# Performance work log

Hardware: AMD Instinct MI355X
Metric: run time of the kernel (lower is better)

Reference implementation:

```python
import jax, jax.numpy as jnp
import numpy as np

B, N, D_MODEL, H, D_K, D_V = 4, 1024, 1024, 16, 64, 1024  # N == D_V required by the module's output matmul


def setup_inputs() -> dict:
    key = jax.random.key(0)
    ks = jax.random.split(key, 7)
    def xavier(k, shape):
        fan_in, fan_out = shape[-2], shape[-1]
        std = (2.0 / (fan_in + fan_out)) ** 0.5
        return jax.random.normal(k, shape, dtype=jnp.float32) * std
    return {
        "query": jax.random.normal(ks[0], (B, N, D_MODEL), dtype=jnp.float32),
        "key": jax.random.normal(ks[1], (B, N, D_MODEL), dtype=jnp.float32),
        "value": jax.random.normal(ks[2], (B, N, D_MODEL), dtype=jnp.float32),
        "w_q": xavier(ks[3], (H, D_MODEL, D_K)),
        "w_k": xavier(ks[4], (H, D_MODEL, D_K)),
        "w_v": xavier(ks[5], (H, D_MODEL, D_V)),
        "w_o": xavier(ks[6], (D_MODEL, H * D_V)),
    }


def reference(query, key, value, w_q, w_k, w_v, w_o):
    # Per-head projections: [B,N,d_model] x [H,d_model,d] -> [B,H,N,d]
    q = jnp.einsum('bnd,hdk->bhnk', query, w_q)
    k = jnp.einsum('bnd,hdk->bhnk', key, w_k)
    v = jnp.einsum('bnd,hdv->bhnv', value, w_v)
    scale = 1.0 / jnp.sqrt(jnp.asarray(q.shape[-1], q.dtype))
    scores = jnp.einsum('bhqk,bhmk->bhqm', q, k) * scale  # [B,H,N,N]
    weights = jax.nn.softmax(scores, axis=-1)
    out = jnp.einsum('bhqm,bhmv->bhqv', weights, v)  # [B,H,N,d_v]
    out = out.reshape(out.shape[0], -1, out.shape[-1])  # [B, H*N, d_v]
    # Faithful to source: torch.matmul(w_o, output) with w_o [d_model, H*d_v];
    # requires H*d_v == H*N (N == d_v); result [B, d_model, d_v].
    return jnp.einsum('de,bev->bdv', w_o, out)
```

## Files before the change

kernel.cpp:

```cpp
#include <hip/hip_runtime.h>
#include <hip/hip_bf16.h>

typedef __hip_bfloat16 bf16;
typedef __attribute__((ext_vector_type(8))) short short8;
typedef __attribute__((ext_vector_type(4))) float floatx4;

#define BK 64
#define LDK 72

__device__ __forceinline__ void gload_lds16(const void* g, void* l) {
    __builtin_amdgcn_global_load_lds(
        (const __attribute__((address_space(1))) void*)g,
        (__attribute__((address_space(3))) void*)l, 16, 0, 0);
}

template<bool OUT_BF16>
__global__ void __launch_bounds__(256) gemm_nt_lds(
    const bf16* __restrict__ A, const bf16* __restrict__ B, void* __restrict__ Cv,
    int M, int N, int K, int lda, int ldb, int ldc,
    long sA, long sB, long sC)
{
    __shared__ __align__(16) bf16 As[128 * 64];
    __shared__ __align__(16) bf16 Bs[128 * 64];

    int bx = blockIdx.x, by = blockIdx.y, bz = blockIdx.z;
    if (gridDim.x == 8 && gridDim.y == 8 && (gridDim.z & 7) == 0) {
        int hw  = bx + (by << 3) + (bz << 6);
        int xcd = hw & 7;
        int idx = hw >> 3;
        int zper = gridDim.z >> 3;
        bz = xcd * zper + (idx >> 6);
        int rem = idx & 63;
        by = rem >> 3;
        bx = rem & 7;
    }

    long aoff = (long)bz * sA;
    long boff = (long)bz * sB;
    long coff = (long)bz * sC;

    int m0 = by * 128;
    int n0 = bx * 128;
    int tid  = threadIdx.x;
    int lane = tid & 63;
    int wave = tid >> 6;
    int quad = lane >> 4;
    int l16  = lane & 15;
    int wm = (wave >> 1) * 64;
    int wn = (wave & 1) * 64;

    int lrow   = lane >> 3;
    int lchunk = (lane & 7) ^ lrow;
    int swz    = l16 & 7;

    const bf16* Abase = A + aoff + (long)m0 * lda;
    const bf16* Bbase = B + boff + (long)n0 * ldb;

    floatx4 acc[4][4] = {};
    const int nt = K / BK;

    for (int kt = 0; kt < nt; kt++) {
        __syncthreads();
        long kofs = (long)kt * BK;
#pragma unroll
        for (int s = 0; s < 4; s++) {
            int r = wave * 32 + s * 8;
            gload_lds16(Abase + (long)(r + lrow) * lda + kofs + lchunk * 8, &As[r * 64]);
            gload_lds16(Bbase + (long)(r + lrow) * ldb + kofs + lchunk * 8, &Bs[r * 64]);
        }
        __syncthreads();

#pragma unroll
        for (int ks = 0; ks < 2; ks++) {
            short8 af[4], bfr[4];
#pragma unroll
            for (int i = 0; i < 4; i++) {
                int ri = wm + i * 16 + l16;
                af[i] = *(const short8*)(&As[ri * 64 + (((ks << 2) | quad) ^ swz) * 8]);
            }
#pragma unroll
            for (int j = 0; j < 4; j++) {
                int rj = wn + j * 16 + l16;
                bfr[j] = *(const short8*)(&Bs[rj * 64 + (((ks << 2) | quad) ^ swz) * 8]);
            }
#pragma unroll
            for (int i = 0; i < 4; i++)
#pragma unroll
                for (int j = 0; j < 4; j++)
                    acc[i][j] = __builtin_amdgcn_mfma_f32_16x16x32_bf16(af[i], bfr[j], acc[i][j], 0, 0, 0);
        }
    }

#pragma unroll
    for (int i = 0; i < 4; i++) {
        int row = m0 + wm + i * 16 + quad * 4;
#pragma unroll
        for (int j = 0; j < 4; j++) {
            int col = n0 + wn + j * 16 + l16;
#pragma unroll
            for (int v = 0; v < 4; v++) {
                int r = row + v;
                float val = acc[i][j][v];
                if (OUT_BF16)
                    ((bf16*)Cv)[coff + (long)r * ldc + col] = __float2bfloat16(val);
                else
                    ((float*)Cv)[coff + (long)r * ldc + col] = val;
            }
        }
    }
}

template<bool OUT_BF16, bool A_F32, bool B_F32>
__global__ void __launch_bounds__(256) gemm_nt(
    const void* __restrict__ Av, const void* __restrict__ Bv, void* __restrict__ Cv,
    int M, int N, int K, int lda, int ldb, int ldc,
    long sA, long sB, long sC)
{
    __shared__ __align__(16) bf16 As[128 * LDK];
    __shared__ __align__(16) bf16 Bs[128 * LDK];

    int bx = blockIdx.x, by = blockIdx.y, bz = blockIdx.z;
    if (gridDim.x == 8 && gridDim.y == 8 && (gridDim.z & 7) == 0) {
        int hw  = bx + (by << 3) + (bz << 6);
        int xcd = hw & 7;
        int idx = hw >> 3;
        int zper = gridDim.z >> 3;
        bz = xcd * zper + (idx >> 6);
        int rem = idx & 63;
        by = rem >> 3;
        bx = rem & 7;
    }

    long aoff = (long)bz * sA;
    long boff = (long)bz * sB;
    long coff = (long)bz * sC;

    int m0 = by * 128;
    int n0 = bx * 128;
    int tid  = threadIdx.x;
    int lane = tid & 63;
    int wave = tid >> 6;
    int quad = lane >> 4;
    int l16  = lane & 15;
    int wm = (wave >> 1) * 64;
    int wn = (wave & 1) * 64;

    int sr = tid >> 3;
    int sc = (tid & 7) * 8;

    floatx4 acc[4][4] = {};

    uint4  pa[4], pb[4];
    float4 pa0[4], pa1[4], pb0[4], pb1[4];

    const int nt = K / BK;

#pragma unroll
    for (int s = 0; s < 4; s++) {
        int r = sr + 32 * s;
        int gm = m0 + r;
        if (A_F32) {
            const float* p = (const float*)Av + aoff + (long)gm * lda + sc;
            if (gm < M) { pa0[s] = *(const float4*)p; pa1[s] = *(const float4*)(p + 4); }
            else { pa0[s] = {0,0,0,0}; pa1[s] = {0,0,0,0}; }
        } else {
            pa[s] = (gm < M) ? *(const uint4*)((const bf16*)Av + aoff + (long)gm * lda + sc)
                             : (uint4){0,0,0,0};
        }
        int gn = n0 + r;
        if (B_F32) {
            const float* p = (const float*)Bv + boff + (long)gn * ldb + sc;
            if (gn < N) { pb0[s] = *(const float4*)p; pb1[s] = *(const float4*)(p + 4); }
            else { pb0[s] = {0,0,0,0}; pb1[s] = {0,0,0,0}; }
        } else {
            pb[s] = (gn < N) ? *(const uint4*)((const bf16*)Bv + boff + (long)gn * ldb + sc)
                             : (uint4){0,0,0,0};
        }
    }

    for (int kt = 0; kt < nt; kt++) {
        __syncthreads();
#pragma unroll
        for (int s = 0; s < 4; s++) {
            int r = sr + 32 * s;
            if (A_F32) {
                bf16 t[8];
                t[0]=__float2bfloat16(pa0[s].x); t[1]=__float2bfloat16(pa0[s].y);
                t[2]=__float2bfloat16(pa0[s].z); t[3]=__float2bfloat16(pa0[s].w);
                t[4]=__float2bfloat16(pa1[s].x); t[5]=__float2bfloat16(pa1[s].y);
                t[6]=__float2bfloat16(pa1[s].z); t[7]=__float2bfloat16(pa1[s].w);
                *(uint4*)(&As[r * LDK + sc]) = *(const uint4*)t;
            } else {
                *(uint4*)(&As[r * LDK + sc]) = pa[s];
            }
            if (B_F32) {
                bf16 t[8];
                t[0]=__float2bfloat16(pb0[s].x); t[1]=__float2bfloat16(pb0[s].y);
                t[2]=__float2bfloat16(pb0[s].z); t[3]=__float2bfloat16(pb0[s].w);
                t[4]=__float2bfloat16(pb1[s].x); t[5]=__float2bfloat16(pb1[s].y);
                t[6]=__float2bfloat16(pb1[s].z); t[7]=__float2bfloat16(pb1[s].w);
                *(uint4*)(&Bs[r * LDK + sc]) = *(const uint4*)t;
            } else {
                *(uint4*)(&Bs[r * LDK + sc]) = pb[s];
            }
        }
        __syncthreads();

        if (kt + 1 < nt) {
            int k0 = (kt + 1) * BK;
#pragma unroll
            for (int s = 0; s < 4; s++) {
                int r = sr + 32 * s;
                int gm = m0 + r;
                if (A_F32) {
                    const float* p = (const float*)Av + aoff + (long)gm * lda + k0 + sc;
                    if (gm < M) { pa0[s] = *(const float4*)p; pa1[s] = *(const float4*)(p + 4); }
                    else { pa0[s] = {0,0,0,0}; pa1[s] = {0,0,0,0}; }
                } else {
                    pa[s] = (gm < M) ? *(const uint4*)((const bf16*)Av + aoff + (long)gm * lda + k0 + sc)
                                     : (uint4){0,0,0,0};
                }
                int gn = n0 + r;
                if (B_F32) {
                    const float* p = (const float*)Bv + boff + (long)gn * ldb + k0 + sc;
                    if (gn < N) { pb0[s] = *(const float4*)p; pb1[s] = *(const float4*)(p + 4); }
                    else { pb0[s] = {0,0,0,0}; pb1[s] = {0,0,0,0}; }
                } else {
                    pb[s] = (gn < N) ? *(const uint4*)((const bf16*)Bv + boff + (long)gn * ldb + k0 + sc)
                                     : (uint4){0,0,0,0};
                }
            }
        }

#pragma unroll
        for (int ks = 0; ks < 2; ks++) {
            short8 af[4], bfr[4];
#pragma unroll
            for (int i = 0; i < 4; i++)
                af[i] = *(const short8*)(&As[(wm + i * 16 + l16) * LDK + ks * 32 + quad * 8]);
#pragma unroll
            for (int j = 0; j < 4; j++)
                bfr[j] = *(const short8*)(&Bs[(wn + j * 16 + l16) * LDK + ks * 32 + quad * 8]);
#pragma unroll
            for (int i = 0; i < 4; i++)
#pragma unroll
                for (int j = 0; j < 4; j++)
                    acc[i][j] = __builtin_amdgcn_mfma_f32_16x16x32_bf16(af[i], bfr[j], acc[i][j], 0, 0, 0);
        }
    }

#pragma unroll
    for (int i = 0; i < 4; i++) {
        int row = m0 + wm + i * 16 + quad * 4;
#pragma unroll
        for (int j = 0; j < 4; j++) {
            int col = n0 + wn + j * 16 + l16;
            if (col >= N) continue;
#pragma unroll
            for (int v = 0; v < 4; v++) {
                int r = row + v;
                if (r < M) {
                    float val = acc[i][j][v];
                    if (OUT_BF16)
                        ((bf16*)Cv)[coff + (long)r * ldc + col] = __float2bfloat16(val);
                    else
                        ((float*)Cv)[coff + (long)r * ldc + col] = val;
                }
            }
        }
    }
}

__global__ void __launch_bounds__(256) attn_softmax(
    const bf16* __restrict__ Q, const bf16* __restrict__ Kb, bf16* __restrict__ Wts)
{
    __shared__ __align__(16) bf16 Ks[64 * 72];

    int h = blockIdx.y;
    const bf16* Qbh = Q  + (long)h * 262144;
    const bf16* Kbh = Kb + (long)h * 262144;
    bf16* W = Wts + (long)h * 1048576;

    int tid  = threadIdx.x;
    int lane = tid & 63;
    int wave = tid >> 6;
    int quad = lane >> 4;
    int l16  = lane & 15;
    int q0 = blockIdx.x * 64 + wave * 16;

    short8 a0 = *(const short8*)(Qbh + (long)(q0 + l16) * 64 + quad * 8);
    short8 a1 = *(const short8*)(Qbh + (long)(q0 + l16) * 64 + 32 + quad * 8);

    int sr = tid >> 3;
    int sc = (tid & 7) * 8;

    const float scale = 0.125f;
    float m_v[4] = {-1e30f, -1e30f, -1e30f, -1e30f};
    float l_v[4] = {0.f, 0.f, 0.f, 0.f};

    for (int t = 0; t < 16; t++) {
        __syncthreads();
        const bf16* src = Kbh + (long)(t * 64 + sr) * 64 + sc;
        *(uint4*)(&Ks[sr * 72 + sc])        = *(const uint4*)src;
        *(uint4*)(&Ks[(sr + 32) * 72 + sc]) = *(const uint4*)(src + 32 * 64);
        __syncthreads();
#pragma unroll
        for (int j = 0; j < 4; j++) {
            short8 b0 = *(const short8*)(&Ks[(j * 16 + l16) * 72 + quad * 8]);
            short8 b1 = *(const short8*)(&Ks[(j * 16 + l16) * 72 + 32 + quad * 8]);
            floatx4 acc = {0.f, 0.f, 0.f, 0.f};
            acc = __builtin_amdgcn_mfma_f32_16x16x32_bf16(a0, b0, acc, 0, 0, 0);
            acc = __builtin_amdgcn_mfma_f32_16x16x32_bf16(a1, b1, acc, 0, 0, 0);
#pragma unroll
            for (int v = 0; v < 4; v++) {
                float s  = acc[v] * scale;
                float nm = fmaxf(m_v[v], s);
                l_v[v] = l_v[v] * __expf(m_v[v] - nm) + __expf(s - nm);
                m_v[v] = nm;
            }
        }
    }

#pragma unroll
    for (int d = 1; d < 16; d <<= 1) {
#pragma unroll
        for (int v = 0; v < 4; v++) {
            float om = __shfl_xor(m_v[v], d);
            float ol = __shfl_xor(l_v[v], d);
            float nm = fmaxf(m_v[v], om);
            l_v[v] = l_v[v] * __expf(m_v[v] - nm) + ol * __expf(om - nm);
            m_v[v] = nm;
        }
    }
    float linv[4];
#pragma unroll
    for (int v = 0; v < 4; v++) linv[v] = 1.0f / l_v[v];

    for (int t = 0; t < 16; t++) {
        __syncthreads();
        const bf16* src = Kbh + (long)(t * 64 + sr) * 64 + sc;
        *(uint4*)(&Ks[sr * 72 + sc])        = *(const uint4*)src;
        *(uint4*)(&Ks[(sr + 32) * 72 + sc]) = *(const uint4*)(src + 32 * 64);
        __syncthreads();
#pragma unroll
        for (int j = 0; j < 4; j++) {
            short8 b0 = *(const short8*)(&Ks[(j * 16 + l16) * 72 + quad * 8]);
            short8 b1 = *(const short8*)(&Ks[(j * 16 + l16) * 72 + 32 + quad * 8]);
            floatx4 acc = {0.f, 0.f, 0.f, 0.f};
            acc = __builtin_amdgcn_mfma_f32_16x16x32_bf16(a0, b0, acc, 0, 0, 0);
            acc = __builtin_amdgcn_mfma_f32_16x16x32_bf16(a1, b1, acc, 0, 0, 0);
#pragma unroll
            for (int v = 0; v < 4; v++) {
                float w = __expf(acc[v] * scale - m_v[v]) * linv[v];
                W[(long)(q0 + quad * 4 + v) * 1024 + t * 64 + j * 16 + l16] = __float2bfloat16(w);
            }
        }
    }
}

__global__ void __launch_bounds__(256) cast_bf16_k(
    const float* __restrict__ in, bf16* __restrict__ out, int n4)
{
    int i = blockIdx.x * 256 + threadIdx.x;
    if (i >= n4) return;
    float4 v = ((const float4*)in)[i];
    bf16 t[4] = {__float2bfloat16(v.x), __float2bfloat16(v.y),
                 __float2bfloat16(v.z), __float2bfloat16(v.w)};
    ((uint2*)out)[i] = *(const uint2*)t;
}

__global__ void __launch_bounds__(256) transpose_cast(
    const float* __restrict__ in, bf16* __restrict__ out, int R, int C)
{
    __shared__ float t[32][33];
    int h = blockIdx.z;
    const float* inh = in + (long)h * R * C;
    bf16* outh = out + (long)h * R * C;
    int c0 = blockIdx.x * 32, r0 = blockIdx.y * 32;
    int tx = threadIdx.x, ty = threadIdx.y;
#pragma unroll
    for (int i = 0; i < 32; i += 8)
        t[ty + i][tx] = inh[(long)(r0 + ty + i) * C + c0 + tx];
    __syncthreads();
#pragma unroll
    for (int i = 0; i < 32; i += 8)
        outh[(long)(c0 + ty + i) * R + r0 + tx] = __float2bfloat16(t[tx][ty + i]);
}

__global__ void __launch_bounds__(256) reduce16_k(
    const float* __restrict__ part, float* __restrict__ out)
{
    int i = blockIdx.x * 256 + threadIdx.x;
    float4 s = ((const float4*)part)[i];
#pragma unroll
    for (int c = 1; c < 16; c++) {
        float4 p = ((const float4*)part)[c * 262144 + i];
        s.x += p.x; s.y += p.y; s.z += p.z; s.w += p.w;
    }
    ((float4*)out)[i] = s;
}

extern "C" void kernel_launch(void* const* d_in, const int* in_sizes, int n_in,
                              void* d_out, int out_size, void* d_ws, size_t ws_size,
                              hipStream_t stream) {
    const float* query = (const float*)d_in[0];
    const float* key   = (const float*)d_in[1];
    const float* value = (const float*)d_in[2];
    const float* w_q   = (const float*)d_in[3];
    const float* w_k   = (const float*)d_in[4];
    const float* w_v   = (const float*)d_in[5];
    const float* w_o   = (const float*)d_in[6];
    float* out = (float*)d_out;

    char* ws = (char*)d_ws;
    const size_t MB = (size_t)1 << 20;
    bf16* wqt      = (bf16*)(ws + 0 * MB);
    bf16* wkt      = (bf16*)(ws + 2 * MB);
    bf16* wvt      = (bf16*)(ws + 4 * MB);
    bf16* wob      = (bf16*)(ws + 36 * MB);
    bf16* qb       = (bf16*)(ws + 68 * MB);
    bf16* kb       = (bf16*)(ws + 76 * MB);
    bf16* vt_b     = (bf16*)(ws + 84 * MB);
    bf16* wts_b    = (bf16*)(ws + 116 * MB);
    bf16* att_b    = (bf16*)(ws + 148 * MB);
    bf16* value_bf = (bf16*)(ws + 148 * MB);
    float* out_part = (float*)(ws + 84 * MB);

    transpose_cast<<<dim3(2, 32, 16),  dim3(32, 8), 0, stream>>>(w_q, wqt, 1024, 64);
    transpose_cast<<<dim3(2, 32, 16),  dim3(32, 8), 0, stream>>>(w_k, wkt, 1024, 64);
    transpose_cast<<<dim3(32, 32, 16), dim3(32, 8), 0, stream>>>(w_v, wvt, 1024, 1024);
    cast_bf16_k<<<16384, 256, 0, stream>>>(w_o, wob, 1024 * 16384 / 4);

    gemm_nt<true, true, false><<<dim3(1, 32, 16), 256, 0, stream>>>(
        query, wqt, qb, 4096, 64, 1024, 1024, 1024, 64, 0L, 65536L, 262144L);
    gemm_nt<true, true, false><<<dim3(1, 32, 16), 256, 0, stream>>>(
        key, wkt, kb, 4096, 64, 1024, 1024, 1024, 64, 0L, 65536L, 262144L);

    for (int b = 0; b < 4; b++) {
        cast_bf16_k<<<1024, 256, 0, stream>>>(value + (long)b * 1048576, value_bf, 262144);

        gemm_nt_lds<true><<<dim3(8, 8, 16), 256, 0, stream>>>(
            wvt, value_bf, vt_b,
            1024, 1024, 1024, 1024, 1024, 1024, 1048576L, 0L, 1048576L);

        attn_softmax<<<dim3(16, 16), 256, 0, stream>>>(
            qb + (long)b * 65536, kb + (long)b * 65536, wts_b);

        gemm_nt_lds<true><<<dim3(8, 8, 16), 256, 0, stream>>>(
            vt_b, wts_b, att_b,
            1024, 1024, 1024, 1024, 1024, 16384, 1048576L, 1048576L, 1024L);

        gemm_nt_lds<false><<<dim3(8, 8, 16), 256, 0, stream>>>(
            wob, att_b, out_part,
            1024, 1024, 1024, 16384, 16384, 1024, 1024L, 1024L, 1048576L);

        reduce16_k<<<1024, 256, 0, stream>>>(out_part, out + (long)b * 1048576);
    }

    (void)in_sizes; (void)n_in; (void)out_size; (void)ws_size;
}
```

Baseline: 1.016 ms.

## Use 256x256 double-buffered GEMM tiles with 512 threads for batched matmuls

Replaces the 128x128 single-buffered LDS GEMM with a 256x256 tile kernel of 8 waves. Each wave now computes 128x64, and the kernel double-buffers LDS so the next K-tile's global-to-LDS loads overlap the MFMAs. It raises MFMA priority with setprio and remaps blocks across XCDs for the new grid. The larger tiles raise data reuse per byte loaded but use 128KB of LDS per block, which gives only one block per CU and 256 blocks per launch. The XCD remap is also removed from the older gemm_nt kernel.

```diff
diff --git a/kernel.cpp b/kernel.cpp
--- a/kernel.cpp
+++ b/kernel.cpp
@@ -15,96 +15,101 @@
 }
 
 template<bool OUT_BF16>
-__global__ void __launch_bounds__(256) gemm_nt_lds(
+__global__ void __launch_bounds__(512) gemm_nt_256(
     const bf16* __restrict__ A, const bf16* __restrict__ B, void* __restrict__ Cv,
-    int M, int N, int K, int lda, int ldb, int ldc,
+    int K, int lda, int ldb, int ldc,
     long sA, long sB, long sC)
 {
-    __shared__ __align__(16) bf16 As[128 * 64];
-    __shared__ __align__(16) bf16 Bs[128 * 64];
+    __shared__ __align__(16) bf16 As[2][256 * 64];
+    __shared__ __align__(16) bf16 Bs[2][256 * 64];
 
     int bx = blockIdx.x, by = blockIdx.y, bz = blockIdx.z;
-    if (gridDim.x == 8 && gridDim.y == 8 && (gridDim.z & 7) == 0) {
-        int hw  = bx + (by << 3) + (bz << 6);
+    if (gridDim.x == 4 && gridDim.y == 4 && (gridDim.z & 7) == 0) {
+        int hw  = bx + (by << 2) + (bz << 4);
         int xcd = hw & 7;
         int idx = hw >> 3;
-        int zper = gridDim.z >> 3;
-        bz = xcd * zper + (idx >> 6);
-        int rem = idx & 63;
-        by = rem >> 3;
-        bx = rem & 7;
-    }
-
-    long aoff = (long)bz * sA;
-    long boff = (long)bz * sB;
+        int per = (int)(gridDim.z >> 3) << 4;
+        int nh  = xcd * per + idx;
+        bx = nh & 3; by = (nh >> 2) & 3; bz = nh >> 4;
+    }
+
+    long aoff = (long)bz * sA + (long)by * 256 * lda;
+    long boff = (long)bz * sB + (long)bx * 256 * ldb;
     long coff = (long)bz * sC;
 
-    int m0 = by * 128;
-    int n0 = bx * 128;
     int tid  = threadIdx.x;
     int lane = tid & 63;
     int wave = tid >> 6;
     int quad = lane >> 4;
     int l16  = lane & 15;
-    int wm = (wave >> 1) * 64;
-    int wn = (wave & 1) * 64;
-
-    int lrow   = lane >> 3;
-    int lchunk = (lane & 7) ^ lrow;
-    int swz    = l16 & 7;
-
-    const bf16* Abase = A + aoff + (long)m0 * lda;
-    const bf16* Bbase = B + boff + (long)n0 * ldb;
-
-    floatx4 acc[4][4] = {};
+    int swz  = l16 & 7;
+    int wm = (wave >> 2) * 128;
+    int wn = (wave & 3) * 64;
+
+    int srow   = tid >> 3;
+    int schunk = (tid & 7) ^ (srow & 7);
+    int dbase  = (wave << 3) * 64;
+
+    const bf16* Asrc = A + aoff;
+    const bf16* Bsrc = B + boff;
+
+    floatx4 acc[8][4] = {};
     const int nt = K / BK;
 
+    auto STAGE = [&](int db, int kt) {
+        long kofs = (long)kt * BK + schunk * 8;
+#pragma unroll
+        for (int s = 0; s < 4; s++) {
+            int r = s * 64 + srow;
+            gload_lds16(Asrc + (long)r * lda + kofs, &As[db][s * 64 * 64 + dbase]);
+            gload_lds16(Bsrc + (long)r * ldb + kofs, &Bs[db][s * 64 * 64 + dbase]);
+        }
+    };
+
+    STAGE(0, 0);
+    __syncthreads();
+
+    int db = 0;
     for (int kt = 0; kt < nt; kt++) {
-        __syncthreads();
-        long kofs = (long)kt * BK;
-#pragma unroll
-        for (int s = 0; s < 4; s++) {
-            int r = wave * 32 + s * 8;
-            gload_lds16(Abase + (long)(r + lrow) * lda + kofs + lchunk * 8, &As[r * 64]);
-            gload_lds16(Bbase + (long)(r + lrow) * ldb + kofs + lchunk * 8, &Bs[r * 64]);
-        }
-        __syncthreads();
+        if (kt + 1 < nt) STAGE(db ^ 1, kt + 1);
+        __builtin_amdgcn_sched_barrier(0);
 
 #pragma unroll
         for (int ks = 0; ks < 2; ks++) {
-            short8 af[4], bfr[4];
-#pragma unroll
-            for (int i = 0; i < 4; i++) {
-                int ri = wm + i * 16 + l16;
-                af[i] = *(const short8*)(&As[ri * 64 + (((ks << 2) | quad) ^ swz) * 8]);
-            }
-#pragma unroll
-            for (int j = 0; j < 4; j++) {
-                int rj = wn + j * 16 + l16;
-                bfr[j] = *(const short8*)(&Bs[rj * 64 + (((ks << 2) | quad) ^ swz) * 8]);
-            }
-#pragma unroll
-            for (int i = 0; i < 4; i++)
+            int cch = ((ks << 2) | quad) ^ swz;
+            short8 af[8], bfr[4];
+#pragma unroll
+            for (int i = 0; i < 8; i++)
+                af[i] = *(const short8*)(&As[db][(wm + i * 16 + l16) * 64 + cch * 8]);
+#pragma unroll
+            for (int j = 0; j < 4; j++)
+                bfr[j] = *(const short8*)(&Bs[db][(wn + j * 16 + l16) * 64 + cch * 8]);
+            __builtin_amdgcn_s_setprio(1);
+#pragma unroll
+            for (int i = 0; i < 8; i++)
 #pragma unroll
                 for (int j = 0; j < 4; j++)
                     acc[i][j] = __builtin_amdgcn_mfma_f32_16x16x32_bf16(af[i], bfr[j], acc[i][j], 0, 0, 0);
-        }
-    }
-
-#pragma unroll
-    for (int i = 0; i < 4; i++) {
-        int row = m0 + wm + i * 16 + quad * 4;
+            __builtin_amdgcn_s_setprio(0);
+        }
+
+        __syncthreads();
+        db ^= 1;
+    }
+
+#pragma unroll
+    for (int i = 0; i < 8; i++) {
+        int row = by * 256 + wm + i * 16 + quad * 4;
 #pragma unroll
         for (int j = 0; j < 4; j++) {
-            int col = n0 + wn + j * 16 + l16;
+            int col = bx * 256 + wn + j * 16 + l16;
 #pragma unroll
             for (int v = 0; v < 4; v++) {
-                int r = row + v;
                 float val = acc[i][j][v];
                 if (OUT_BF16)
-                    ((bf16*)Cv)[coff + (long)r * ldc + col] = __float2bfloat16(val);
+                    ((bf16*)Cv)[coff + (long)(row + v) * ldc + col] = __float2bfloat16(val);
                 else
-                    ((float*)Cv)[coff + (long)r * ldc + col] = val;
+                    ((float*)Cv)[coff + (long)(row + v) * ldc + col] = val;
             }
         }
     }
@@ -120,16 +125,6 @@
     __shared__ __align__(16) bf16 Bs[128 * LDK];
 
     int bx = blockIdx.x, by = blockIdx.y, bz = blockIdx.z;
-    if (gridDim.x == 8 && gridDim.y == 8 && (gridDim.z & 7) == 0) {
-        int hw  = bx + (by << 3) + (bz << 6);
-        int xcd = hw & 7;
-        int idx = hw >> 3;
-        int zper = gridDim.z >> 3;
-        bz = xcd * zper + (idx >> 6);
-        int rem = idx & 63;
-        by = rem >> 3;
-        bx = rem & 7;
-    }
 
     long aoff = (long)bz * sA;
     long boff = (long)bz * sB;
@@ -439,20 +434,20 @@
     for (int b = 0; b < 4; b++) {
         cast_bf16_k<<<1024, 256, 0, stream>>>(value + (long)b * 1048576, value_bf, 262144);
 
-        gemm_nt_lds<true><<<dim3(8, 8, 16), 256, 0, stream>>>(
+        gemm_nt_256<true><<<dim3(4, 4, 16), 512, 0, stream>>>(
             wvt, value_bf, vt_b,
-            1024, 1024, 1024, 1024, 1024, 1024, 1048576L, 0L, 1048576L);
+            1024, 1024, 1024, 1024, 1048576L, 0L, 1048576L);
 
         attn_softmax<<<dim3(16, 16), 256, 0, stream>>>(
             qb + (long)b * 65536, kb + (long)b * 65536, wts_b);
 
-        gemm_nt_lds<true><<<dim3(8, 8, 16), 256, 0, stream>>>(
+        gemm_nt_256<true><<<dim3(4, 4, 16), 512, 0, stream>>>(
             vt_b, wts_b, att_b,
-            1024, 1024, 1024, 1024, 1024, 16384, 1048576L, 1048576L, 1024L);
-
-        gemm_nt_lds<false><<<dim3(8, 8, 16), 256, 0, stream>>>(
+            1024, 1024, 1024, 16384, 1048576L, 1048576L, 1024L);
+
+        gemm_nt_256<false><<<dim3(4, 4, 16), 512, 0, stream>>>(
             wob, att_b, out_part,
-            1024, 1024, 1024, 16384, 16384, 1024, 1024L, 1024L, 1048576L);
+            1024, 16384, 16384, 1024, 1024L, 1024L, 1048576L);
 
         reduce16_k<<<1024, 256, 0, stream>>>(out_part, out + (long)b * 1048576);
     }
```

New measurement: 911.2 us. 10.3% less time.
